# Optimization experiments

Measured on AMD Instinct MI355X. Metric: run time of the kernel, lower is better.

## Reference

```python
import jax, jax.numpy as jnp
import numpy as np

B, C, COUT, L, K = 16, 64, 64, 16384, 3
STRIDE, PAD, DIL, G, DG = 1, 1, 1, 1, 1
LOUT = (L + 2 * PAD - DIL * (K - 1) - 1) // STRIDE + 1


def _conv1d(x, w, b, pad, groups):
    # x: [B, Cin, L], w: [Cout, Cin/groups, k] (torch Conv1d layout)
    y = jax.lax.conv_general_dilated(
        x, w, window_strides=(1,), padding=[(pad, pad)],
        dimension_numbers=('NCH', 'OIH', 'NCH'), feature_group_count=groups)
    return y + b[None, :, None]


def setup_inputs() -> dict:
    key = jax.random.key(0)
    k = jax.random.split(key, 11)
    s = jnp.float32(0.02)  # module init: normal(0, 0.02)
    return {
        'x': jax.random.normal(k[0], (B, C, L), jnp.float32),
        'w_off_dw': jax.random.normal(k[1], (C, 1, 7), jnp.float32) * s,
        'b_off_dw': jax.random.normal(k[2], (C,), jnp.float32) * s,
        'w_off_pw': jax.random.normal(k[3], (G * DG * K, C, 1), jnp.float32) * s,
        'b_off_pw': jax.random.normal(k[4], (G * DG * K,), jnp.float32) * s,
        'w_msk_dw': jax.random.normal(k[5], (C, 1, 7), jnp.float32) * s,
        'b_msk_dw': jax.random.normal(k[6], (C,), jnp.float32) * s,
        'w_msk_pw': jax.random.normal(k[7], (G * DG * K, C, 1), jnp.float32) * s,
        'b_msk_pw': jax.random.normal(k[8], (G * DG * K,), jnp.float32) * s,
        'weight': jax.random.normal(k[9], (COUT, C // G, K), jnp.float32) * s,
        'bias': jax.random.normal(k[10], (COUT,), jnp.float32) * s,
    }


def _deform_conv1d(x, w_off_dw, b_off_dw, w_off_pw, b_off_pw,
                   w_msk_dw, b_msk_dw, w_msk_pw, b_msk_pw, weight, bias):
    # offset / modulation-mask branches: depthwise k=7 conv -> 1x1 conv
    offset = _conv1d(_conv1d(x, w_off_dw, b_off_dw, 3, C), w_off_pw, b_off_pw, 0, 1)  # [B, G*DG*K, Lout]
    mask = jax.nn.sigmoid(_conv1d(_conv1d(x, w_msk_dw, b_msk_dw, 3, C), w_msk_pw, b_msk_pw, 0, 1))

    cpd = C // (G * DG)  # channels per deformable group
    off = jnp.repeat(offset.reshape(B, G * DG, K, LOUT), cpd, axis=1)  # [B, C, K, Lout]
    msk = jnp.repeat(mask.reshape(B, G * DG, K, LOUT), cpd, axis=1)

    base = jnp.arange(LOUT, dtype=x.dtype) * STRIDE - PAD  # [Lout]
    kpos = jnp.arange(K, dtype=x.dtype) * DIL              # [K]
    p = base[None, :] + kpos[:, None]                       # [K, Lout]
    p = p[None, None] + off                                 # fractional sample positions [B, C, K, Lout]

    i0 = jnp.floor(p)
    frac = p - i0
    i0i = i0.astype(jnp.int32)
    i1i = i0i + 1

    xb = jnp.broadcast_to(x[:, :, None, :], (B, C, K, L))
    x0 = jnp.take_along_axis(xb, jnp.clip(i0i, 0, L - 1), axis=-1)
    x1 = jnp.take_along_axis(xb, jnp.clip(i1i, 0, L - 1), axis=-1)
    v0 = ((i0i >= 0) & (i0i < L)).astype(x.dtype)  # zero padding outside
    v1 = ((i1i >= 0) & (i1i < L)).astype(x.dtype)

    # linear interpolation + mask modulation
    val = ((1.0 - frac) * x0 * v0 + frac * x1 * v1) * msk  # [B, C, K, Lout]

    # grouped contraction over (in-channels-per-group, kernel taps)
    out = jnp.einsum('bgikl,goik->bgol',
                     val.reshape(B, G, C // G, K, LOUT),
                     weight.reshape(G, COUT // G, C // G, K))
    return out.reshape(B, COUT, LOUT) + bias[None, :, None]


def reference(x, w_off_dw, b_off_dw, w_off_pw, b_off_pw,
              w_msk_dw, b_msk_dw, w_msk_pw, b_msk_pw, weight, bias):
    return _deform_conv1d(x, w_off_dw, b_off_dw, w_off_pw, b_off_pw,
                          w_msk_dw, b_msk_dw, w_msk_pw, b_msk_pw, weight, bias)
```

## Files before the change

kernel.cpp:

```cpp
#include <hip/hip_runtime.h>
#include <cstdint>

#define LX 16384
#define NB 16
#define LT 64
#define TPB 4
#define HALO 8
#define XI (LT + 2*HALO)
#define XPD 36

typedef __attribute__((ext_vector_type(2))) _Float16 h2;
typedef __attribute__((ext_vector_type(8))) _Float16 h8;
typedef __attribute__((ext_vector_type(4))) unsigned u4;
typedef __attribute__((ext_vector_type(4))) float f4;

static __device__ __forceinline__ h2 u2h(unsigned u) {
    union { unsigned u; h2 h; } v; v.u = u; return v.h;
}
static __device__ __forceinline__ unsigned h2u(h2 h) {
    union { h2 h; unsigned u; } v; v.h = h; return v.u;
}
static __device__ __forceinline__ unsigned pkrtz(float a, float b) {
    auto r = __builtin_amdgcn_cvt_pkrtz(a, b);
    union { decltype(r) h; unsigned u; } v; v.h = r;
    return v.u;
}

#define BAR_LGKM() do { asm volatile("s_waitcnt lgkmcnt(0)" ::: "memory"); \
                        __builtin_amdgcn_s_barrier();                      \
                        asm volatile("" ::: "memory"); } while (0)
#define BAR_RAW()  do { asm volatile("" ::: "memory");                     \
                        __builtin_amdgcn_s_barrier();                      \
                        asm volatile("" ::: "memory"); } while (0)

__global__ void prep_kernel(const float* __restrict__ weight,
                            const float* __restrict__ b_off_pw, const float* __restrict__ w_off_pw,
                            const float* __restrict__ b_off_dw,
                            const float* __restrict__ b_msk_pw, const float* __restrict__ w_msk_pw,
                            const float* __restrict__ b_msk_dw,
                            const float* __restrict__ w_off_dw, const float* __restrict__ w_msk_dw,
                            short* __restrict__ A2, float* __restrict__ beff,
                            unsigned* __restrict__ wcg) {
    int bid = blockIdx.x;
    int t = threadIdx.x;
    if (bid < 48) {
        int idx = bid * 256 + t;
        int o = idx / 192;
        int rem = idx - o * 192;
        int tap = rem >> 6, c = rem & 63;
        union { _Float16 h; short s; } v;
        v.h = (_Float16)weight[o * 192 + c * 3 + tap];
        A2[idx] = v.s;
    } else {
        int lane = t >> 2, d = t & 3;
        int m = lane & 15, qq = lane >> 4;
        #pragma unroll
        for (int s = 0; s < 14; ++s) {
            int j = s >> 1;
            int c = (s & 1) * 32 + qq * 8 + 2 * d;
            float w0 = 0.f, w1 = 0.f;
            if (m < 3) {
                w0 = w_off_pw[m * 64 + c]     * w_off_dw[c * 7 + j];
                w1 = w_off_pw[m * 64 + c + 1] * w_off_dw[(c + 1) * 7 + j];
            } else if (m < 6) {
                w0 = w_msk_pw[(m - 3) * 64 + c]     * w_msk_dw[c * 7 + j];
                w1 = w_msk_pw[(m - 3) * 64 + c + 1] * w_msk_dw[(c + 1) * 7 + j];
            }
            wcg[s * 256 + t] = pkrtz(w0, w1);
        }
        if (t < 6) {
            int br = t / 3, m3 = t % 3;
            const float* pw = br ? w_msk_pw : w_off_pw;
            const float* bd = br ? b_msk_dw : b_off_dw;
            const float* bp = br ? b_msk_pw : b_off_pw;
            float s = bp[m3];
            for (int c = 0; c < 64; ++c) s += pw[m3 * 64 + c] * bd[c];
            beff[t] = s;
        }
    }
}

__launch_bounds__(256, 4)
__global__ void deform_main(const float* __restrict__ x,
                            const float* __restrict__ bias,
                            const short* __restrict__ A2,
                            const float* __restrict__ beff,
                            const unsigned* __restrict__ wcg,
                            float* __restrict__ out) {
    __shared__ __align__(16) unsigned xdw[XI * XPD];
    __shared__ __align__(16) unsigned A2l[6144];
    __shared__ float bias_l[64];
    __shared__ float beff_l[8];

    const int t = threadIdx.x;
    const int lane = t & 63;
    const int wv = t >> 6;
    const int r = lane & 15, q = lane >> 4;
    const int lbase = blockIdx.x * (LT * TPB);
    const int b = blockIdx.y;
    const float* xb = x + (size_t)b * (64 * LX);

    f4 rx0[3], rx1[3];

    auto issue_x = [&](int l0v) {
        #pragma unroll
        for (int s = 0; s < 3; ++s) {
            int p = t + 256 * s;
            rx0[s] = (f4){0.f, 0.f, 0.f, 0.f};
            rx1[s] = (f4){0.f, 0.f, 0.f, 0.f};
            if (p < 640) {
                int cp = p & 31, up = p >> 5;
                int g4 = l0v - HALO + up * 4;
                if ((unsigned)g4 < (unsigned)LX) {
                    rx0[s] = *(const f4*)(xb + (size_t)(2 * cp) * LX + g4);
                    rx1[s] = *(const f4*)(xb + (size_t)(2 * cp + 1) * LX + g4);
                }
            }
        }
    };
    auto write_x = [&]() {
        #pragma unroll
        for (int s = 0; s < 3; ++s) {
            int p = t + 256 * s;
            if (p < 640) {
                int cp = p & 31, up = p >> 5;
                #pragma unroll
                for (int d = 0; d < 4; ++d) {
                    int i = up * 4 + d;
                    int pc = ((cp >> 3) + i) & 3;
                    xdw[i * XPD + pc * 8 + (cp & 7)] = pkrtz(rx0[s][d], rx1[s][d]);
                }
            }
        }
    };

    issue_x(lbase);
    {
        const u4* A2g4 = (const u4*)A2;
        #pragma unroll
        for (int s = 0; s < 6; ++s) {
            int idx = t + 256 * s;
            int row = idx / 24;
            int g = idx - row * 24;
            int pdw = row * 96 + ((g * 4) ^ ((row & 7) << 2));
            *(u4*)&A2l[pdw] = A2g4[idx];
        }
    }
    if (t < 64) bias_l[t] = bias[t];
    if (t < 6)  beff_l[t] = beff[t];
    write_x();
    BAR_LGKM();

    #pragma unroll
    for (int tt = 0; tt < TPB; ++tt) {
        const int l0 = lbase + tt * LT;

        const u4* wcp = (const u4*)wcg;
        asm volatile("" : "+s"(wcp));
        u4 wfr[14];
        #pragma unroll
        for (int s = 0; s < 14; ++s) wfr[s] = wcp[s * 64 + lane];

        unsigned mywp = 0; int myli = 0;
        {
            f4 acc2a = {0.f, 0.f, 0.f, 0.f};
            f4 acc2b = {0.f, 0.f, 0.f, 0.f};
            const int irow = wv * 16 + r + 5;
            #pragma unroll
            for (int s = 0; s < 14; ++s) {
                const int j = s >> 1, half = s & 1;
                const int i = irow + j;
                const int chunk = half * 2 + (q >> 1);
                const int pd = i * XPD + (((chunk + i) & 3) << 3) + ((q & 1) << 2);
                union { u4 u; h8 h; } bx; bx.u = *(const u4*)&xdw[pd];
                union { u4 u; h8 h; } ax; ax.u = wfr[s];
                if (s & 1)
                    acc2b = __builtin_amdgcn_mfma_f32_16x16x32_f16(ax.h, bx.h, acc2b, 0, 0, 0);
                else
                    acc2a = __builtin_amdgcn_mfma_f32_16x16x32_f16(ax.h, bx.h, acc2a, 0, 0, 0);
            }
            f4 acc2 = acc2a + acc2b;
            float b0 = __shfl(acc2[0], r);
            float b1 = __shfl(acc2[1], r);
            float b2 = __shfl(acc2[2], r);
            float m0 = __shfl(acc2[3], r);
            float m1 = __shfl(acc2[0], 16 + r);
            float m2 = __shfl(acc2[1], 16 + r);
            if (q < 3) {
                const int k = q, l = wv * 16 + r;
                float off = (k == 0 ? b0 : k == 1 ? b1 : b2) + beff_l[k];
                float z   = (k == 0 ? m0 : k == 1 ? m1 : m2) + beff_l[3 + k];
                float msk = 1.0f / (1.0f + __expf(-z));
                float p = (float)(l0 + l - 1 + k) + off;
                float fl = floorf(p);
                int i0 = (int)fl, i1 = i0 + 1;
                float fr = p - fl;
                int li0 = i0 - l0 + HALO, li1 = li0 + 1;
                float w0 = (((unsigned)i0 < (unsigned)LX) && ((unsigned)li0 < (unsigned)XI)) ? (1.0f - fr) * msk : 0.0f;
                float w1 = (((unsigned)i1 < (unsigned)LX) && ((unsigned)li1 < (unsigned)XI)) ? fr * msk : 0.0f;
                li0 = min(max(li0, 0), XI - 2);
                mywp = pkrtz(w0, w1);
                myli = li0;
            }
        }

        if (tt + 1 < TPB) issue_x(l0 + LT);

        {
            const int lcol = wv * 16 + r;
            unsigned wpt[3]; int lit[3];
            #pragma unroll
            for (int tap = 0; tap < 3; ++tap) {
                wpt[tap] = __shfl(mywp, tap * 16 + r);
                lit[tap] = __shfl(myli, tap * 16 + r);
            }
            f4 acc[4];
            #pragma unroll
            for (int mt = 0; mt < 4; ++mt) acc[mt] = (f4){0.f, 0.f, 0.f, 0.f};
            const int sw = (r & 7) << 2;
            #pragma unroll
            for (int kk = 0; kk < 6; ++kk) {
                const int tap = kk >> 1;
                unsigned wp = wpt[tap];
                unsigned w00 = __builtin_amdgcn_perm(wp, wp, 0x01000100u);
                unsigned w11 = __builtin_amdgcn_perm(wp, wp, 0x03020302u);
                int li0 = lit[tap];
                int cp0 = ((kk & 1) << 4) + (q << 2);
                int chunkL = cp0 >> 3;
                int o0 = li0 * XPD + ((((chunkL + li0) & 3) << 3) | (cp0 & 7));
                int o1 = (li0 + 1) * XPD + ((((chunkL + li0 + 1) & 3) << 3) | (cp0 & 7));
                u4 r0 = *(const u4*)&xdw[o0];
                u4 r1 = *(const u4*)&xdw[o1];
                u4 xs;
                #pragma unroll
                for (int d = 0; d < 4; ++d)
                    xs[d] = h2u(u2h(r0[d]) * u2h(w00) + u2h(r1[d]) * u2h(w11));
                union { u4 u; h8 h; } bfr; bfr.u = xs;
                #pragma unroll
                for (int mt = 0; mt < 4; ++mt) {
                    union { u4 u; h8 h; } af;
                    af.u = *(const u4*)&A2l[(mt * 16 + r) * 96 + ((kk * 16 + q * 4) ^ sw)];
                    acc[mt] = __builtin_amdgcn_mfma_f32_16x16x32_f16(af.h, bfr.h, acc[mt], 0, 0, 0);
                }
            }
            #pragma unroll
            for (int mt = 0; mt < 4; ++mt) {
                int ob = mt * 16 + 4 * q;
                float* op = out + ((size_t)b * 64 + ob) * LX + l0 + lcol;
                #pragma unroll
                for (int e = 0; e < 4; ++e)
                    op[(size_t)e * LX] = acc[mt][e] + bias_l[ob + e];
            }
        }

        if (tt < TPB - 1) {
            BAR_RAW();
            write_x();
            BAR_LGKM();
        }
    }
}

extern "C" void kernel_launch(void* const* d_in, const int* in_sizes, int n_in,
                              void* d_out, int out_size, void* d_ws, size_t ws_size,
                              hipStream_t stream) {
    const float* x        = (const float*)d_in[0];
    const float* w_off_dw = (const float*)d_in[1];
    const float* b_off_dw = (const float*)d_in[2];
    const float* w_off_pw = (const float*)d_in[3];
    const float* b_off_pw = (const float*)d_in[4];
    const float* w_msk_dw = (const float*)d_in[5];
    const float* b_msk_dw = (const float*)d_in[6];
    const float* w_msk_pw = (const float*)d_in[7];
    const float* b_msk_pw = (const float*)d_in[8];
    const float* weight   = (const float*)d_in[9];
    const float* bias     = (const float*)d_in[10];
    float* out = (float*)d_out;

    short*    A2   = (short*)d_ws;
    float*    beff = (float*)((char*)d_ws + 24576);
    unsigned* wcg  = (unsigned*)((char*)d_ws + 24608);

    hipLaunchKernelGGL(prep_kernel, dim3(49), dim3(256), 0, stream,
                       weight, b_off_pw, w_off_pw, b_off_dw, b_msk_pw, w_msk_pw, b_msk_dw,
                       w_off_dw, w_msk_dw, A2, beff, wcg);
    hipLaunchKernelGGL(deform_main, dim3(LX / (LT * TPB), NB), dim3(256), 0, stream,
                       x, bias, A2, beff, wcg, out);
}
```

Before: 165.6 us.

## Double-buffer LDS x tile, hoist weight fragments, halve tiles per block

Gives the x tile in LDS two buffers, so the next tile can be written while the current one is still being read. This removes the pre-write barrier that each tile iteration needed before. The per-lane offset/mask weight fragments are now loaded once before the tile loop instead of once per tile. Tiles per block drop from 4 to 2, which doubles the grid, and the launch-bounds occupancy hint is lowered from 4 to 3 to fit the larger LDS footprint. The costs are more LDS per block, possibly fewer resident blocks, and more redundant A2 staging across the larger grid.

Measured after the change: 149.4 us. 1.11x faster.

```diff
diff --git a/kernel.cpp b/kernel.cpp
--- a/kernel.cpp
+++ b/kernel.cpp
@@ -4,10 +4,11 @@
 #define LX 16384
 #define NB 16
 #define LT 64
-#define TPB 4
+#define TPB 2
 #define HALO 8
 #define XI (LT + 2*HALO)
 #define XPD 36
+#define XSZ (XI * XPD)
 
 typedef __attribute__((ext_vector_type(2))) _Float16 h2;
 typedef __attribute__((ext_vector_type(8))) _Float16 h8;
@@ -27,9 +28,6 @@
 }
 
 #define BAR_LGKM() do { asm volatile("s_waitcnt lgkmcnt(0)" ::: "memory"); \
-                        __builtin_amdgcn_s_barrier();                      \
-                        asm volatile("" ::: "memory"); } while (0)
-#define BAR_RAW()  do { asm volatile("" ::: "memory");                     \
                         __builtin_amdgcn_s_barrier();                      \
                         asm volatile("" ::: "memory"); } while (0)
 
@@ -80,14 +78,14 @@
     }
 }
 
-__launch_bounds__(256, 4)
+__launch_bounds__(256, 3)
 __global__ void deform_main(const float* __restrict__ x,
                             const float* __restrict__ bias,
                             const short* __restrict__ A2,
                             const float* __restrict__ beff,
                             const unsigned* __restrict__ wcg,
                             float* __restrict__ out) {
-    __shared__ __align__(16) unsigned xdw[XI * XPD];
+    __shared__ __align__(16) unsigned xdw[2 * XSZ];
     __shared__ __align__(16) unsigned A2l[6144];
     __shared__ float bias_l[64];
     __shared__ float beff_l[8];
@@ -118,7 +116,7 @@
             }
         }
     };
-    auto write_x = [&]() {
+    auto write_x = [&](unsigned base) {
         #pragma unroll
         for (int s = 0; s < 3; ++s) {
             int p = t + 256 * s;
@@ -128,7 +126,7 @@
                 for (int d = 0; d < 4; ++d) {
                     int i = up * 4 + d;
                     int pc = ((cp >> 3) + i) & 3;
-                    xdw[i * XPD + pc * 8 + (cp & 7)] = pkrtz(rx0[s][d], rx1[s][d]);
+                    xdw[base + i * XPD + pc * 8 + (cp & 7)] = pkrtz(rx0[s][d], rx1[s][d]);
                 }
             }
         }
@@ -146,20 +144,22 @@
             *(u4*)&A2l[pdw] = A2g4[idx];
         }
     }
+    u4 wfr[14];
+    {
+        const u4* wc4 = (const u4*)wcg;
+        #pragma unroll
+        for (int s = 0; s < 14; ++s) wfr[s] = wc4[s * 64 + lane];
+    }
     if (t < 64) bias_l[t] = bias[t];
     if (t < 6)  beff_l[t] = beff[t];
-    write_x();
+    write_x(0);
     BAR_LGKM();
 
     #pragma unroll
     for (int tt = 0; tt < TPB; ++tt) {
         const int l0 = lbase + tt * LT;
-
-        const u4* wcp = (const u4*)wcg;
-        asm volatile("" : "+s"(wcp));
-        u4 wfr[14];
-        #pragma unroll
-        for (int s = 0; s < 14; ++s) wfr[s] = wcp[s * 64 + lane];
+        const unsigned cur = (unsigned)(tt & 1) * XSZ;
+        const unsigned nxt = (unsigned)((tt + 1) & 1) * XSZ;
 
         unsigned mywp = 0; int myli = 0;
         {
@@ -171,7 +171,7 @@
                 const int j = s >> 1, half = s & 1;
                 const int i = irow + j;
                 const int chunk = half * 2 + (q >> 1);
-                const int pd = i * XPD + (((chunk + i) & 3) << 3) + ((q & 1) << 2);
+                const int pd = cur + i * XPD + (((chunk + i) & 3) << 3) + ((q & 1) << 2);
                 union { u4 u; h8 h; } bx; bx.u = *(const u4*)&xdw[pd];
                 union { u4 u; h8 h; } ax; ax.u = wfr[s];
                 if (s & 1)
@@ -227,8 +227,8 @@
                 int li0 = lit[tap];
                 int cp0 = ((kk & 1) << 4) + (q << 2);
                 int chunkL = cp0 >> 3;
-                int o0 = li0 * XPD + ((((chunkL + li0) & 3) << 3) | (cp0 & 7));
-                int o1 = (li0 + 1) * XPD + ((((chunkL + li0 + 1) & 3) << 3) | (cp0 & 7));
+                int o0 = cur + li0 * XPD + ((((chunkL + li0) & 3) << 3) | (cp0 & 7));
+                int o1 = cur + (li0 + 1) * XPD + ((((chunkL + li0 + 1) & 3) << 3) | (cp0 & 7));
                 u4 r0 = *(const u4*)&xdw[o0];
                 u4 r1 = *(const u4*)&xdw[o1];
                 u4 xs;
@@ -254,8 +254,7 @@
         }
 
         if (tt < TPB - 1) {
-            BAR_RAW();
-            write_x();
+            write_x(nxt);
             BAR_LGKM();
         }
     }
```
